# Kernel tuning notes

Hardware: AMD Instinct MI355X
Metric: run time of the kernel (lower is better)

Reference implementation:

```python
import jax, jax.numpy as jnp
import numpy as np

D_MODEL = 512
N_HEADS = 8
D_KV = 64
EPS = 1e-6
ROPE_THETA = 10000.0


def _rms_norm(x, w):
    # T5-style RMSNorm: no mean subtraction, no bias, variance in fp32.
    var = jnp.mean(x.astype(jnp.float32) ** 2, axis=-1, keepdims=True)
    return (x * jax.lax.rsqrt(var + EPS)).astype(x.dtype) * w


def _rope_cos_sin(pos, dk):
    # pos: [B, T] int -> cos/sin: [B, 1, T, dk]
    inv_freq = 1.0 / (ROPE_THETA ** (jnp.arange(0, dk, 2, dtype=jnp.float32) / dk))
    ang = pos.astype(jnp.float32)[:, :, None] * inv_freq[None, None, :]  # [B,T,dk/2]
    ang = jnp.concatenate([ang, ang], axis=-1)                            # [B,T,dk]
    return jnp.cos(ang)[:, None], jnp.sin(ang)[:, None]


def _rotate_half(x):
    h = x.shape[-1] // 2
    return jnp.concatenate([-x[..., h:], x[..., :h]], axis=-1)


def _mha(x, mask, wq, wk, wv, wo, pos=None):
    # x: [B, T, D]; mask: [B, H, T, T] additive
    B, T, _ = x.shape
    def proj(w):
        return (x @ w).reshape(B, T, N_HEADS, D_KV).transpose(0, 2, 1, 3)  # [B,H,T,dk]
    q, k, v = proj(wq), proj(wk), proj(wv)
    if pos is not None:
        cos, sin = _rope_cos_sin(pos, D_KV)
        cos, sin = cos.astype(x.dtype), sin.astype(x.dtype)
        q = q * cos + _rotate_half(q) * sin
        k = k * cos + _rotate_half(k) * sin
    scale = 1.0 / np.sqrt(D_KV)
    scores = jnp.einsum('bhqd,bhkd->bhqk', q, k) * scale + mask
    attn = jax.nn.softmax(scores.astype(jnp.float32), axis=-1).astype(scores.dtype)
    out = jnp.einsum('bhqk,bhkd->bhqd', attn, v)
    out = out.transpose(0, 2, 1, 3).reshape(B, T, N_HEADS * D_KV)
    return out @ wo


def setup_inputs() -> dict:
    key = jax.random.key(0)
    ks = jax.random.split(key, 12)
    B, T = 8, 1024
    s = 1.0 / np.sqrt(D_MODEL)
    inp = {
        'h': jax.random.normal(ks[0], (B, T, D_MODEL), dtype=jnp.float32),
        'pos': jnp.broadcast_to(jnp.arange(T, dtype=jnp.int64 if jax.config.jax_enable_x64 else jnp.int32)[None, :], (B, T)),
        't_mask': jnp.zeros((B, N_HEADS, T, T), dtype=jnp.float32),
        'g_mask': jnp.zeros((T, N_HEADS, B, B), dtype=jnp.float32),
        'ln_t_w': jnp.ones((D_MODEL,), dtype=jnp.float32),
        'ln_g_w': jnp.ones((D_MODEL,), dtype=jnp.float32),
    }
    names = ['wq_t', 'wk_t', 'wv_t', 'wo_t', 'wq_g', 'wk_g', 'wv_g', 'wo_g']
    for i, n in enumerate(names):
        inp[n] = jax.random.normal(ks[i + 1], (D_MODEL, D_MODEL), dtype=jnp.float32) * s
    return inp


def reference(h, pos, t_mask, g_mask, ln_t_w, ln_g_w,
              wq_t, wk_t, wv_t, wo_t, wq_g, wk_g, wv_g, wo_g):
    # --- time attention (over T axis, with RoPE) ---
    normed = _rms_norm(h, ln_t_w)
    attn_t = _mha(normed, t_mask, wq_t, wk_t, wv_t, wo_t, pos=pos)
    h = h + attn_t  # dropout p=0 (eval)
    # --- group attention (over B axis, no RoPE) ---
    h = h.transpose(1, 0, 2)  # [T, B, D]
    normed = _rms_norm(h, ln_g_w)
    attn_g = _mha(normed, g_mask, wq_g, wk_g, wv_g, wo_g, pos=None)
    h = h + attn_g
    return h.transpose(1, 0, 2)  # back to [B, T, D]
```

## Files before the change

kernel.cpp:

```cpp
#include <hip/hip_runtime.h>
#include <hip/hip_bf16.h>
#include <math.h>


typedef __bf16 bf16x8 __attribute__((ext_vector_type(8)));
typedef __bf16 bf16x4 __attribute__((ext_vector_type(4)));
typedef float  f32x4  __attribute__((ext_vector_type(4)));

#define LN1E4_OVER_32 0.2878231366242558f

__device__ __forceinline__ void gld16(const void* g, void* l) {
    __builtin_amdgcn_global_load_lds((const __attribute__((address_space(1))) void*)g,
                                     (__attribute__((address_space(3))) void*)l,
                                     16, 0, 0);
}

__device__ __forceinline__ int swz64(int r, int c) {
    return r * 64 + (((c + r) & 7) << 3);
}

__global__ __launch_bounds__(256) void prep_k(
    const float* __restrict__ x, const float* __restrict__ wln, __bf16* __restrict__ y,
    const float* w0, const float* w1, const float* w2, const float* w3,
    const float* w4, const float* w5, const float* w6, const float* w7,
    const float* __restrict__ gln, float* __restrict__ rmsbuf,
    __bf16* qkvT_t, __bf16* oT_t, __bf16* qkvT_g, __bf16* oT_g,
    const int* __restrict__ pos, float2* __restrict__ rope)
{
    __shared__ float tile[32][33];
    int bid = blockIdx.x;
    if (bid < 2048) {
        if (bid < 32) rmsbuf[bid * 256 + threadIdx.x] = 0.0f;
        int row = bid * 4 + (threadIdx.x >> 6);
        int l = threadIdx.x & 63;
        const float* xr = x + (size_t)row * 512 + l * 8;
        float4 a = *(const float4*)xr;
        float4 b = *(const float4*)(xr + 4);
        float ss = a.x*a.x + a.y*a.y + a.z*a.z + a.w*a.w
                 + b.x*b.x + b.y*b.y + b.z*b.z + b.w*b.w;
        for (int m = 1; m < 64; m <<= 1) ss += __shfl_xor(ss, m);
        float rms = rsqrtf(ss * (1.0f / 512.0f) + 1e-6f);
        float4 wa = *(const float4*)(wln + l * 8);
        float4 wb = *(const float4*)(wln + l * 8 + 4);
        bf16x8 o;
        o[0] = (__bf16)(a.x * rms * wa.x); o[1] = (__bf16)(a.y * rms * wa.y);
        o[2] = (__bf16)(a.z * rms * wa.z); o[3] = (__bf16)(a.w * rms * wa.w);
        o[4] = (__bf16)(b.x * rms * wb.x); o[5] = (__bf16)(b.y * rms * wb.y);
        o[6] = (__bf16)(b.z * rms * wb.z); o[7] = (__bf16)(b.w * rms * wb.w);
        *(bf16x8*)(y + (size_t)row * 512 + l * 8) = o;
        return;
    }
    if (bid >= 4096) {
        int idx = bid - 4096;
        int r = threadIdx.x >> 5, i = threadIdx.x & 31;
        int row = idx * 8 + r;
        float p = (float)pos[row];
        float f = __expf((float)i * -LN1E4_OVER_32);
        float s, c;
        __sincosf(p * f, &s, &c);
        rope[(size_t)row * 32 + i] = make_float2(c, s);
        return;
    }
    int bid2 = bid - 2048;
    int mat = bid2 >> 8, rem = bid2 & 255;
    const float* src; __bf16* dst; int rowOff;
    switch (mat) {
        case 0: src=w0; dst=qkvT_t; rowOff=0;    break;
        case 1: src=w1; dst=qkvT_t; rowOff=512;  break;
        case 2: src=w2; dst=qkvT_t; rowOff=1024; break;
        case 3: src=w3; dst=oT_t;   rowOff=0;    break;
        case 4: src=w4; dst=qkvT_g; rowOff=0;    break;
        case 5: src=w5; dst=qkvT_g; rowOff=512;  break;
        case 6: src=w6; dst=qkvT_g; rowOff=1024; break;
        default: src=w7; dst=oT_g;  rowOff=0;    break;
    }
    bool foldG = (mat >= 4 && mat <= 6);
    int n0 = (rem & 15) * 32, k0 = (rem >> 4) * 32;
    int tt = threadIdx.x;
    int kr = tt >> 3, nc = (tt & 7) * 4;
    float4 v = *(const float4*)(src + (size_t)(k0 + kr) * 512 + n0 + nc);
    tile[kr][nc+0] = v.x; tile[kr][nc+1] = v.y; tile[kr][nc+2] = v.z; tile[kr][nc+3] = v.w;
    __syncthreads();
    int nr = tt >> 3, kc = (tt & 7) * 4;
    float g0 = 1.f, g1 = 1.f, g2 = 1.f, g3 = 1.f;
    if (foldG) {
        float4 gv = *(const float4*)(gln + k0 + kc);
        g0 = gv.x; g1 = gv.y; g2 = gv.z; g3 = gv.w;
    }
    bf16x4 o;
    o[0] = (__bf16)(tile[kc+0][nr] * g0); o[1] = (__bf16)(tile[kc+1][nr] * g1);
    o[2] = (__bf16)(tile[kc+2][nr] * g2); o[3] = (__bf16)(tile[kc+3][nr] * g3);
    *(bf16x4*)(dst + (size_t)(rowOff + n0 + nr) * 512 + k0 + kc) = o;
}

__global__ __launch_bounds__(256) void gemm_ep(
    const __bf16* __restrict__ A, const __bf16* __restrict__ Bt,
    const float2* __restrict__ rope, const float* __restrict__ rmsv,
    __bf16* __restrict__ o0, __bf16* __restrict__ o1, __bf16* __restrict__ o2,
    int mode)
{
    __shared__ __bf16 smem[16384];
    __bf16* As = smem;
    __bf16* Bs = smem + 8192;
    int tid = threadIdx.x;
    int l = tid & 63, w = tid >> 6;
    int l16 = l & 15, quad = l >> 4;
    int wm = w >> 1, wn = w & 1;
    int mblk = blockIdx.x * 128, nblk = blockIdx.y * 128;
    f32x4 acc[4][4] = {};

    for (int k0 = 0; k0 < 512; k0 += 64) {
        __syncthreads();
        #pragma unroll
        for (int i = 0; i < 4; ++i) {
            int idx = i * 256 + tid;
            int row = idx >> 3, cp = idx & 7;
            int cl = (cp - row) & 7;
            gld16(A  + (size_t)(mblk + row) * 512 + k0 + cl * 8, (char*)As + (size_t)idx * 16);
            gld16(Bt + (size_t)(nblk + row) * 512 + k0 + cl * 8, (char*)Bs + (size_t)idx * 16);
        }
        __syncthreads();
        #pragma unroll
        for (int h = 0; h < 2; h++) {
            bf16x8 aF[4], bF[4];
            #pragma unroll
            for (int mt = 0; mt < 4; mt++) aF[mt] = *(bf16x8*)(As + swz64(wm * 64 + mt * 16 + l16, h * 4 + quad));
            #pragma unroll
            for (int nt = 0; nt < 4; nt++) bF[nt] = *(bf16x8*)(Bs + swz64(wn * 64 + nt * 16 + l16, h * 4 + quad));
            #pragma unroll
            for (int mt = 0; mt < 4; mt++)
                #pragma unroll
                for (int nt = 0; nt < 4; nt++)
                    acc[mt][nt] = __builtin_amdgcn_mfma_f32_16x16x32_bf16(aF[mt], bF[nt], acc[mt][nt], 0, 0, 0);
        }
    }
    __syncthreads();

    int colbase = nblk + wn * 64;
    __bf16* bw = smem + w * 1536;
    int rbrow = l >> 3, rbch = (l & 7) * 8;

    int mat = colbase >> 9;
    int hh  = (colbase & 511) >> 6;
    __bf16* dst = (mat == 0) ? o0 : (mat == 1) ? o1 : o2;
    bool isQ = (mat == 0), isV = (mat == 2);
    if (mode == 0 && !isV) {
        #pragma unroll
        for (int mt = 0; mt < 4; mt++) {
            int grow0 = mblk + wm * 64 + mt * 16;
            int b = grow0 >> 10, t0 = grow0 & 1023;
            #pragma unroll
            for (int r = 0; r < 4; r++) {
                const float2* tp = rope + (size_t)(grow0 + quad * 4 + r) * 32;
                #pragma unroll
                for (int nt = 0; nt < 2; nt++) {
                    int i = nt * 16 + l16;
                    float2 cs = tp[i];
                    float x1 = acc[mt][nt][r], x2 = acc[mt][nt + 2][r];
                    float y1 = x1 * cs.x - x2 * cs.y;
                    float y2 = x2 * cs.x + x1 * cs.y;
                    if (isQ) { y1 *= 0.125f; y2 *= 0.125f; }
                    bw[(quad * 4 + r) * 72 + i]      = (__bf16)y1;
                    bw[(quad * 4 + r) * 72 + i + 32] = (__bf16)y2;
                }
            }
            #pragma unroll
            for (int i = 0; i < 2; ++i) {
                int rr = rbrow + i * 8;
                bf16x8 vv = *(bf16x8*)&bw[rr * 72 + rbch];
                *(bf16x8*)&dst[((size_t)(b * 8 + hh) * 1024 + t0 + rr) * 64 + rbch] = vv;
            }
        }
    } else if (mode == 0) {
        #pragma unroll
        for (int mt = 0; mt < 4; mt++) {
            #pragma unroll
            for (int nt = 0; nt < 4; nt++) {
                bf16x4 o4;
                #pragma unroll
                for (int r = 0; r < 4; r++) o4[r] = (__bf16)acc[mt][nt][r];
                *(bf16x4*)&bw[(nt * 16 + l16) * 24 + quad * 4] = o4;
            }
            int grow0 = mblk + wm * 64 + mt * 16;
            int b = grow0 >> 10, t0 = grow0 & 1023;
            #pragma unroll
            for (int i = 0; i < 2; ++i) {
                int li = i * 64 + l;
                int d = li >> 1, t8 = (li & 1) * 8;
                bf16x8 vv = *(bf16x8*)&bw[d * 24 + t8];
                *(bf16x8*)&dst[((size_t)(b * 8 + hh) * 64 + d) * 1024 + t0 + t8] = vv;
            }
        }
    } else {
        #pragma unroll
        for (int mt = 0; mt < 4; mt++) {
            int grow0 = mblk + wm * 64 + mt * 16;
            f32x4 ss4 = *(const f32x4*)&rmsv[grow0 + quad * 4];
            float rsq[4];
            #pragma unroll
            for (int r = 0; r < 4; r++)
                rsq[r] = rsqrtf(ss4[r] * (1.0f / 512.0f) + 1e-6f) * (isQ ? 0.125f : 1.0f);
            #pragma unroll
            for (int nt = 0; nt < 4; nt++)
                #pragma unroll
                for (int r = 0; r < 4; r++)
                    bw[(quad * 4 + r) * 72 + nt * 16 + l16] = (__bf16)(acc[mt][nt][r] * rsq[r]);
            #pragma unroll
            for (int i = 0; i < 2; ++i) {
                int rr = rbrow + i * 8;
                int grow = grow0 + rr;
                int t = grow >> 3, bq = grow & 7;
                bf16x8 vv = *(bf16x8*)&bw[rr * 72 + rbch];
                *(bf16x8*)&dst[(((size_t)t * 8 + hh) * 8 + bq) * 64 + rbch] = vv;
            }
        }
    }
}

__global__ __launch_bounds__(256) void gemm_o(
    const __bf16* __restrict__ A, const __bf16* __restrict__ Bt,
    const float* __restrict__ resid, float* __restrict__ outF,
    __bf16* __restrict__ h2b, float* __restrict__ rmsbuf, int remap)
{
    __shared__ __align__(16) char smemraw[24576];
    __bf16* As = (__bf16*)smemraw;
    __bf16* Bs = (__bf16*)(smemraw + 8192);
    int tid = threadIdx.x;
    int l = tid & 63, w = tid >> 6;
    int l16 = l & 15, quad = l >> 4;
    int mblk = blockIdx.x * 64, nblk = blockIdx.y * 128;
    f32x4 acc[8] = {};

    for (int k0 = 0; k0 < 512; k0 += 64) {
        __syncthreads();
        #pragma unroll
        for (int i = 0; i < 2; ++i) {
            int idx = i * 256 + tid;
            int row = idx >> 3, cp = idx & 7;
            int cl = (cp - row) & 7;
            gld16(A + (size_t)(mblk + row) * 512 + k0 + cl * 8, (char*)As + (size_t)idx * 16);
        }
        #pragma unroll
        for (int i = 0; i < 4; ++i) {
            int idx = i * 256 + tid;
            int row = idx >> 3, cp = idx & 7;
            int cl = (cp - row) & 7;
            gld16(Bt + (size_t)(nblk + row) * 512 + k0 + cl * 8, (char*)Bs + (size_t)idx * 16);
        }
        __syncthreads();
        #pragma unroll
        for (int h = 0; h < 2; h++) {
            bf16x8 aF = *(bf16x8*)(As + swz64(w * 16 + l16, h * 4 + quad));
            #pragma unroll
            for (int nt = 0; nt < 8; nt++) {
                bf16x8 bF = *(bf16x8*)(Bs + swz64(nt * 16 + l16, h * 4 + quad));
                acc[nt] = __builtin_amdgcn_mfma_f32_16x16x32_bf16(aF, bF, acc[nt], 0, 0, 0);
            }
        }
    }
    __syncthreads();

    float* fw = (float*)(smemraw + w * 4352);
    int grow0 = mblk + w * 16;
    float ssq[4] = {0.f, 0.f, 0.f, 0.f};
    #pragma unroll
    for (int nh = 0; nh < 2; nh++) {
        #pragma unroll
        for (int nt = 0; nt < 4; nt++)
            #pragma unroll
            for (int r = 0; r < 4; r++)
                fw[(quad * 4 + r) * 68 + nt * 16 + l16] = acc[nh * 4 + nt][r];
        #pragma unroll
        for (int i = 0; i < 4; ++i) {
            int rr = i * 4 + (l >> 4);
            int c4 = (l & 15) * 4;
            f32x4 a4 = *(f32x4*)&fw[rr * 68 + c4];
            int grow = grow0 + rr;
            int orow = remap ? (((grow & 7) << 10) + (grow >> 3)) : grow;
            size_t oi = (size_t)orow * 512 + nblk + nh * 64 + c4;
            f32x4 r4 = *(const f32x4*)&resid[oi];
            r4 += a4;
            *(f32x4*)&outF[oi] = r4;
            if (!remap) {
                int b = grow >> 10, t = grow & 1023;
                int orow2 = t * 8 + b;
                bf16x4 h4;
                h4[0] = (__bf16)r4[0]; h4[1] = (__bf16)r4[1];
                h4[2] = (__bf16)r4[2]; h4[3] = (__bf16)r4[3];
                *(bf16x4*)&h2b[(size_t)orow2 * 512 + nblk + nh * 64 + c4] = h4;
                ssq[i] += r4[0]*r4[0] + r4[1]*r4[1] + r4[2]*r4[2] + r4[3]*r4[3];
            }
        }
    }
    if (!remap) {
        #pragma unroll
        for (int i = 0; i < 4; ++i) {
            float s = ssq[i];
            s += __shfl_xor(s, 1);
            s += __shfl_xor(s, 2);
            s += __shfl_xor(s, 4);
            s += __shfl_xor(s, 8);
            if ((l & 15) == 0) {
                int grow = grow0 + i * 4 + (l >> 4);
                int orow2 = (grow & 1023) * 8 + (grow >> 10);
                atomicAdd(&rmsbuf[orow2], s);
            }
        }
    }
}

__global__ __launch_bounds__(512) void flash_t(
    const __bf16* __restrict__ q, const __bf16* __restrict__ k,
    const __bf16* __restrict__ vt, const float* __restrict__ tmask,
    __bf16* __restrict__ ctx)
{
    int bh = blockIdx.x;
    int w = threadIdx.x >> 6, l = threadIdx.x & 63;
    int l16 = l & 15, quad = l >> 4;
    int q0 = blockIdx.y * 128 + w * 16;

    __shared__ __bf16 Ks[64 * 72];
    __shared__ __bf16 Vs[64 * 72];
    __shared__ __bf16 Ps[8][16 * 72];

    bf16x8 aQ0, aQ1;
    {
        const __bf16* qp = q + ((size_t)bh * 1024 + q0 + l16) * 64 + quad * 8;
        aQ0 = *(const bf16x8*)qp;
        aQ1 = *(const bf16x8*)(qp + 32);
    }
    f32x4 o[4] = {};
    float l_acc[4] = {0.0f, 0.0f, 0.0f, 0.0f};

    const float* mrow = tmask + (size_t)bh * 1024 * 1024 + (size_t)(q0 + quad * 4) * 1024 + l16;
    float mc[16];
    #pragma unroll
    for (int r = 0; r < 4; r++)
        #pragma unroll
        for (int nt = 0; nt < 4; nt++)
            mc[r * 4 + nt] = __builtin_nontemporal_load(mrow + (size_t)r * 1024 + nt * 16);

    int c = threadIdx.x;
    int srow = c >> 3, scol = (c & 7) << 3;
    const __bf16* kbase = k  + ((size_t)bh * 1024 + srow) * 64 + scol;
    const __bf16* vbase = vt + ((size_t)bh * 64 + srow) * 1024 + scol;
    bf16x8 kreg = *(const bf16x8*)kbase;
    bf16x8 vreg = *(const bf16x8*)vbase;

    for (int jb = 0; jb < 1024; jb += 64) {
        __syncthreads();
        *(bf16x8*)&Ks[srow * 72 + scol] = kreg;
        *(bf16x8*)&Vs[srow * 72 + scol] = vreg;
        __syncthreads();
        if (jb + 64 < 1024) {
            kreg = *(const bf16x8*)(kbase + (size_t)(jb + 64) * 64);
            vreg = *(const bf16x8*)(vbase + (jb + 64));
        }

        float mn_[16];
        {
            int jb2 = (jb + 64) & 1023;
            const float* mr2 = mrow + jb2;
            #pragma unroll
            for (int r = 0; r < 4; r++)
                #pragma unroll
                for (int nt = 0; nt < 4; nt++)
                    mn_[r * 4 + nt] = __builtin_nontemporal_load(mr2 + (size_t)r * 1024 + nt * 16);
        }

        f32x4 s[4] = {};
        #pragma unroll
        for (int nt = 0; nt < 4; nt++) {
            bf16x8 b0 = *(bf16x8*)&Ks[(nt * 16 + l16) * 72 + quad * 8];
            bf16x8 b1 = *(bf16x8*)&Ks[(nt * 16 + l16) * 72 + 32 + quad * 8];
            s[nt] = __builtin_amdgcn_mfma_f32_16x16x32_bf16(aQ0, b0, s[nt], 0, 0, 0);
            s[nt] = __builtin_amdgcn_mfma_f32_16x16x32_bf16(aQ1, b1, s[nt], 0, 0, 0);
        }
        #pragma unroll
        for (int r = 0; r < 4; r++)
            #pragma unroll
            for (int nt = 0; nt < 4; nt++) {
                float p = __expf(s[nt][r] + mc[r * 4 + nt]);
                s[nt][r] = p;
                l_acc[r] += p;
            }

        __bf16* ps = Ps[w];
        #pragma unroll
        for (int nt = 0; nt < 4; nt++)
            #pragma unroll
            for (int r = 0; r < 4; r++)
                ps[(quad * 4 + r) * 72 + nt * 16 + l16] = (__bf16)s[nt][r];
        bf16x8 aP0 = *(bf16x8*)&ps[l16 * 72 + quad * 8];
        bf16x8 aP1 = *(bf16x8*)&ps[l16 * 72 + 32 + quad * 8];
        #pragma unroll
        for (int dt = 0; dt < 4; dt++) {
            bf16x8 bv0 = *(bf16x8*)&Vs[(dt * 16 + l16) * 72 + quad * 8];
            bf16x8 bv1 = *(bf16x8*)&Vs[(dt * 16 + l16) * 72 + 32 + quad * 8];
            o[dt] = __builtin_amdgcn_mfma_f32_16x16x32_bf16(aP0, bv0, o[dt], 0, 0, 0);
            o[dt] = __builtin_amdgcn_mfma_f32_16x16x32_bf16(aP1, bv1, o[dt], 0, 0, 0);
        }

        #pragma unroll
        for (int i = 0; i < 16; i++) mc[i] = mn_[i];
    }

    float inv_l[4];
    #pragma unroll
    for (int r = 0; r < 4; r++) {
        float rs = l_acc[r];
        rs += __shfl_xor(rs, 1);
        rs += __shfl_xor(rs, 2);
        rs += __shfl_xor(rs, 4);
        rs += __shfl_xor(rs, 8);
        inv_l[r] = 1.0f / rs;
    }

    int b = bh >> 3, h = bh & 7;
    __bf16* ps = Ps[w];
    #pragma unroll
    for (int dt = 0; dt < 4; dt++)
        #pragma unroll
        for (int r = 0; r < 4; r++)
            ps[(quad * 4 + r) * 72 + dt * 16 + l16] = (__bf16)(o[dt][r] * inv_l[r]);
    int rbrow = l >> 3, rbch = (l & 7) * 8;
    #pragma unroll
    for (int i = 0; i < 2; ++i) {
        int rr = rbrow + i * 8;
        bf16x8 vv = *(bf16x8*)&ps[rr * 72 + rbch];
        *(bf16x8*)&ctx[((size_t)b * 1024 + q0 + rr) * 512 + h * 64 + rbch] = vv;
    }
}

__global__ __launch_bounds__(256) void group_attn(
    const __bf16* __restrict__ qg, const __bf16* __restrict__ kg,
    const __bf16* __restrict__ vg, const float* __restrict__ gmask,
    __bf16* __restrict__ ctxg)
{
    int tid = blockIdx.x * 256 + threadIdx.x;
    int t = tid >> 6, h = (tid >> 3) & 7, bq = tid & 7;
    size_t base = ((size_t)t * 8 + h) * 512;

    float qv[64];
    #pragma unroll
    for (int d0 = 0; d0 < 64; d0 += 8) {
        bf16x8 qq = *(const bf16x8*)&qg[base + (size_t)bq * 64 + d0];
        #pragma unroll
        for (int u = 0; u < 8; u++) qv[d0 + u] = (float)qq[u];
    }
    float s[8];
    #pragma unroll
    for (int j = 0; j < 8; j++) {
        float acc = 0.0f;
        #pragma unroll
        for (int d0 = 0; d0 < 64; d0 += 8) {
            bf16x8 kk = *(const bf16x8*)&kg[base + (size_t)j * 64 + d0];
            #pragma unroll
            for (int u = 0; u < 8; u++) acc += qv[d0 + u] * (float)kk[u];
        }
        s[j] = acc + gmask[(((size_t)t * 8 + h) * 8 + bq) * 8 + j];
    }
    float mx = s[0];
    #pragma unroll
    for (int j = 1; j < 8; j++) mx = fmaxf(mx, s[j]);
    float sum = 0.0f;
    #pragma unroll
    for (int j = 0; j < 8; j++) { s[j] = __expf(s[j] - mx); sum += s[j]; }
    float inv = 1.0f / sum;

    #pragma unroll
    for (int d0 = 0; d0 < 64; d0 += 8) {
        float o8[8] = {};
        #pragma unroll
        for (int j = 0; j < 8; j++) {
            bf16x8 vv = *(const bf16x8*)&vg[base + (size_t)j * 64 + d0];
            float pj = s[j];
            #pragma unroll
            for (int u = 0; u < 8; u++) o8[u] += pj * (float)vv[u];
        }
        bf16x8 ob;
        #pragma unroll
        for (int u = 0; u < 8; u++) ob[u] = (__bf16)(o8[u] * inv);
        *(bf16x8*)&ctxg[((size_t)t * 8 + bq) * 512 + h * 64 + d0] = ob;
    }
}

extern "C" void kernel_launch(void* const* d_in, const int* in_sizes, int n_in,
                              void* d_out, int out_size, void* d_ws, size_t ws_size,
                              hipStream_t stream)
{
    const float* h      = (const float*)d_in[0];
    const int*   pos    = (const int*)  d_in[1];
    const float* t_mask = (const float*)d_in[2];
    const float* g_mask = (const float*)d_in[3];
    const float* ln_t_w = (const float*)d_in[4];
    const float* ln_g_w = (const float*)d_in[5];
    const float* wq_t = (const float*)d_in[6];
    const float* wk_t = (const float*)d_in[7];
    const float* wv_t = (const float*)d_in[8];
    const float* wo_t = (const float*)d_in[9];
    const float* wq_g = (const float*)d_in[10];
    const float* wk_g = (const float*)d_in[11];
    const float* wv_g = (const float*)d_in[12];
    const float* wo_g = (const float*)d_in[13];
    float* out = (float*)d_out;

    char* ws = (char*)d_ws;
    const size_t MB = 1ull << 20;
    __bf16* qkvT_t = (__bf16*)ws;
    __bf16* oT_t   = qkvT_t + 786432;
    __bf16* qkvT_g = qkvT_t + 1048576;
    __bf16* oT_g   = qkvT_t + 1835008;
    __bf16* normed = (__bf16*)(ws + 4 * MB);
    __bf16* qb     = (__bf16*)(ws + 12 * MB);
    __bf16* kb     = (__bf16*)(ws + 20 * MB);
    __bf16* vb     = (__bf16*)(ws + 28 * MB);
    __bf16* ctx    = (__bf16*)(ws + 36 * MB);
    float*  h2     = (float*) (ws + 44 * MB);
    float*  rmsbuf = (float*) (ws + 60 * MB);
    __bf16* h2b    = (__bf16*)(ws + 61 * MB);
    float2* rope   = (float2*)(ws + 70 * MB);

    prep_k<<<5120, 256, 0, stream>>>(h, ln_t_w, normed,
        wq_t, wk_t, wv_t, wo_t, wq_g, wk_g, wv_g, wo_g,
        ln_g_w, rmsbuf, qkvT_t, oT_t, qkvT_g, oT_g, pos, rope);
    gemm_ep<<<dim3(64, 12), 256, 0, stream>>>(normed, qkvT_t, rope, nullptr, qb, kb, vb, 0);
    flash_t<<<dim3(64, 8), 512, 0, stream>>>(qb, kb, vb, t_mask, ctx);
    gemm_o<<<dim3(128, 4), 256, 0, stream>>>(ctx, oT_t, h, h2, h2b, rmsbuf, 0);

    gemm_ep<<<dim3(64, 12), 256, 0, stream>>>(h2b, qkvT_g, nullptr, rmsbuf, qb, kb, vb, 2);
    group_attn<<<256, 256, 0, stream>>>(qb, kb, vb, g_mask, ctx);
    gemm_o<<<dim3(128, 4), 256, 0, stream>>>(ctx, oT_g, h2, out, nullptr, nullptr, 1);
}
```

Measured before the change: 496.7 us.

## Enlarge QKV GEMM tiles with double-buffered LDS pipeline and retile output GEMM

The QKV projection GEMM moves to 256x256 block tiles with 512 threads. It double-buffers 64-wide K slices in LDS, overlapping global-to-LDS loads with MFMA work using explicit vmcnt waits, barriers and s_setprio around the MFMA bursts. The output-projection GEMM switches from 64x128 tiles with 4 warps sharing the N dimension to 128x128 tiles in a 2x2 warp grid, and does the RMS partial-sum reduction per sub-tile with more atomics. Larger tiles cut redundant operand loads, but they also shrink the grids (192 and 256 blocks), which may leave compute units idle. The 128 KB LDS per block also limits occupancy.

```diff
diff --git a/kernel.cpp b/kernel.cpp
--- a/kernel.cpp
+++ b/kernel.cpp
@@ -93,45 +93,82 @@
     *(bf16x4*)(dst + (size_t)(rowOff + n0 + nr) * 512 + k0 + kc) = o;
 }
 
-__global__ __launch_bounds__(256) void gemm_ep(
+__global__ __launch_bounds__(512) void gemm_ep(
     const __bf16* __restrict__ A, const __bf16* __restrict__ Bt,
     const float2* __restrict__ rope, const float* __restrict__ rmsv,
     __bf16* __restrict__ o0, __bf16* __restrict__ o1, __bf16* __restrict__ o2,
     int mode)
 {
-    __shared__ __bf16 smem[16384];
-    __bf16* As = smem;
-    __bf16* Bs = smem + 8192;
+    __shared__ __bf16 smem[65536];
     int tid = threadIdx.x;
     int l = tid & 63, w = tid >> 6;
     int l16 = l & 15, quad = l >> 4;
-    int wm = w >> 1, wn = w & 1;
-    int mblk = blockIdx.x * 128, nblk = blockIdx.y * 128;
-    f32x4 acc[4][4] = {};
-
-    for (int k0 = 0; k0 < 512; k0 += 64) {
-        __syncthreads();
+    int wm = w >> 2, wn = w & 3;
+    int mblk = blockIdx.x * 256, nblk = blockIdx.y * 256;
+    f32x4 acc[8][4] = {};
+
+    auto stage = [&](int kt, int bb) {
+        int k0 = kt * 64;
+        __bf16* As = smem + bb * 32768;
+        __bf16* Bs = As + 16384;
         #pragma unroll
         for (int i = 0; i < 4; ++i) {
-            int idx = i * 256 + tid;
+            int idx = i * 512 + tid;
             int row = idx >> 3, cp = idx & 7;
             int cl = (cp - row) & 7;
-            gld16(A  + (size_t)(mblk + row) * 512 + k0 + cl * 8, (char*)As + (size_t)idx * 16);
+            gld16(A + (size_t)(mblk + row) * 512 + k0 + cl * 8, (char*)As + (size_t)idx * 16);
+        }
+        #pragma unroll
+        for (int i = 0; i < 4; ++i) {
+            int idx = i * 512 + tid;
+            int row = idx >> 3, cp = idx & 7;
+            int cl = (cp - row) & 7;
             gld16(Bt + (size_t)(nblk + row) * 512 + k0 + cl * 8, (char*)Bs + (size_t)idx * 16);
         }
-        __syncthreads();
-        #pragma unroll
-        for (int h = 0; h < 2; h++) {
-            bf16x8 aF[4], bF[4];
-            #pragma unroll
-            for (int mt = 0; mt < 4; mt++) aF[mt] = *(bf16x8*)(As + swz64(wm * 64 + mt * 16 + l16, h * 4 + quad));
-            #pragma unroll
-            for (int nt = 0; nt < 4; nt++) bF[nt] = *(bf16x8*)(Bs + swz64(wn * 64 + nt * 16 + l16, h * 4 + quad));
-            #pragma unroll
-            for (int mt = 0; mt < 4; mt++)
+    };
+
+    stage(0, 0);
+    stage(1, 1);
+    asm volatile("s_waitcnt vmcnt(8)" ::: "memory");
+    __builtin_amdgcn_s_barrier();
+    __builtin_amdgcn_sched_barrier(0);
+
+    #pragma unroll 1
+    for (int t = 0; t < 8; ++t) {
+        const __bf16* As = smem + (t & 1) * 32768;
+        const __bf16* Bs = As + 16384;
+        bf16x8 bF[4][2];
+        #pragma unroll
+        for (int nt = 0; nt < 4; nt++)
+            #pragma unroll
+            for (int h = 0; h < 2; h++)
+                bF[nt][h] = *(const bf16x8*)(Bs + swz64(wn * 64 + nt * 16 + l16, h * 4 + quad));
+        #pragma unroll
+        for (int p = 0; p < 4; p++) {
+            bf16x8 aF[2][2];
+            #pragma unroll
+            for (int m2 = 0; m2 < 2; m2++)
+                #pragma unroll
+                for (int h = 0; h < 2; h++)
+                    aF[m2][h] = *(const bf16x8*)(As + swz64(wm * 128 + (p * 2 + m2) * 16 + l16, h * 4 + quad));
+            __builtin_amdgcn_s_setprio(1);
+            #pragma unroll
+            for (int m2 = 0; m2 < 2; m2++)
                 #pragma unroll
                 for (int nt = 0; nt < 4; nt++)
-                    acc[mt][nt] = __builtin_amdgcn_mfma_f32_16x16x32_bf16(aF[mt], bF[nt], acc[mt][nt], 0, 0, 0);
+                    #pragma unroll
+                    for (int h = 0; h < 2; h++)
+                        acc[p * 2 + m2][nt] = __builtin_amdgcn_mfma_f32_16x16x32_bf16(
+                            aF[m2][h], bF[nt][h], acc[p * 2 + m2][nt], 0, 0, 0);
+            __builtin_amdgcn_s_setprio(0);
+        }
+        __builtin_amdgcn_s_barrier();
+        if (t < 6) stage(t + 2, t & 1);
+        if (t < 7) {
+            if (t < 6) asm volatile("s_waitcnt vmcnt(8)" ::: "memory");
+            else       asm volatile("s_waitcnt vmcnt(0)" ::: "memory");
+            __builtin_amdgcn_s_barrier();
+            __builtin_amdgcn_sched_barrier(0);
         }
     }
     __syncthreads();
@@ -146,8 +183,8 @@
     bool isQ = (mat == 0), isV = (mat == 2);
     if (mode == 0 && !isV) {
         #pragma unroll
-        for (int mt = 0; mt < 4; mt++) {
-            int grow0 = mblk + wm * 64 + mt * 16;
+        for (int mt = 0; mt < 8; mt++) {
+            int grow0 = mblk + wm * 128 + mt * 16;
             int b = grow0 >> 10, t0 = grow0 & 1023;
             #pragma unroll
             for (int r = 0; r < 4; r++) {
@@ -173,7 +210,7 @@
         }
     } else if (mode == 0) {
         #pragma unroll
-        for (int mt = 0; mt < 4; mt++) {
+        for (int mt = 0; mt < 8; mt++) {
             #pragma unroll
             for (int nt = 0; nt < 4; nt++) {
                 bf16x4 o4;
@@ -181,7 +218,7 @@
                 for (int r = 0; r < 4; r++) o4[r] = (__bf16)acc[mt][nt][r];
                 *(bf16x4*)&bw[(nt * 16 + l16) * 24 + quad * 4] = o4;
             }
-            int grow0 = mblk + wm * 64 + mt * 16;
+            int grow0 = mblk + wm * 128 + mt * 16;
             int b = grow0 >> 10, t0 = grow0 & 1023;
             #pragma unroll
             for (int i = 0; i < 2; ++i) {
@@ -193,8 +230,8 @@
         }
     } else {
         #pragma unroll
-        for (int mt = 0; mt < 4; mt++) {
-            int grow0 = mblk + wm * 64 + mt * 16;
+        for (int mt = 0; mt < 8; mt++) {
+            int grow0 = mblk + wm * 128 + mt * 16;
             f32x4 ss4 = *(const f32x4*)&rmsv[grow0 + quad * 4];
             float rsq[4];
             #pragma unroll
@@ -222,54 +259,52 @@
     const float* __restrict__ resid, float* __restrict__ outF,
     __bf16* __restrict__ h2b, float* __restrict__ rmsbuf, int remap)
 {
-    __shared__ __align__(16) char smemraw[24576];
+    __shared__ __align__(16) char smemraw[32768];
     __bf16* As = (__bf16*)smemraw;
-    __bf16* Bs = (__bf16*)(smemraw + 8192);
+    __bf16* Bs = (__bf16*)(smemraw + 16384);
     int tid = threadIdx.x;
     int l = tid & 63, w = tid >> 6;
     int l16 = l & 15, quad = l >> 4;
-    int mblk = blockIdx.x * 64, nblk = blockIdx.y * 128;
-    f32x4 acc[8] = {};
+    int wm = w >> 1, wn = w & 1;
+    int mblk = blockIdx.x * 128, nblk = blockIdx.y * 128;
+    f32x4 acc[4][4] = {};
 
     for (int k0 = 0; k0 < 512; k0 += 64) {
         __syncthreads();
-        #pragma unroll
-        for (int i = 0; i < 2; ++i) {
-            int idx = i * 256 + tid;
-            int row = idx >> 3, cp = idx & 7;
-            int cl = (cp - row) & 7;
-            gld16(A + (size_t)(mblk + row) * 512 + k0 + cl * 8, (char*)As + (size_t)idx * 16);
-        }
         #pragma unroll
         for (int i = 0; i < 4; ++i) {
             int idx = i * 256 + tid;
             int row = idx >> 3, cp = idx & 7;
             int cl = (cp - row) & 7;
+            gld16(A  + (size_t)(mblk + row) * 512 + k0 + cl * 8, (char*)As + (size_t)idx * 16);
             gld16(Bt + (size_t)(nblk + row) * 512 + k0 + cl * 8, (char*)Bs + (size_t)idx * 16);
         }
         __syncthreads();
         #pragma unroll
         for (int h = 0; h < 2; h++) {
-            bf16x8 aF = *(bf16x8*)(As + swz64(w * 16 + l16, h * 4 + quad));
-            #pragma unroll
-            for (int nt = 0; nt < 8; nt++) {
-                bf16x8 bF = *(bf16x8*)(Bs + swz64(nt * 16 + l16, h * 4 + quad));
-                acc[nt] = __builtin_amdgcn_mfma_f32_16x16x32_bf16(aF, bF, acc[nt], 0, 0, 0);
-            }
+            bf16x8 aF[4], bF[4];
+            #pragma unroll
+            for (int mt = 0; mt < 4; mt++) aF[mt] = *(bf16x8*)(As + swz64(wm * 64 + mt * 16 + l16, h * 4 + quad));
+            #pragma unroll
+            for (int nt = 0; nt < 4; nt++) bF[nt] = *(bf16x8*)(Bs + swz64(wn * 64 + nt * 16 + l16, h * 4 + quad));
+            #pragma unroll
+            for (int mt = 0; mt < 4; mt++)
+                #pragma unroll
+                for (int nt = 0; nt < 4; nt++)
+                    acc[mt][nt] = __builtin_amdgcn_mfma_f32_16x16x32_bf16(aF[mt], bF[nt], acc[mt][nt], 0, 0, 0);
         }
     }
     __syncthreads();
 
     float* fw = (float*)(smemraw + w * 4352);
-    int grow0 = mblk + w * 16;
-    float ssq[4] = {0.f, 0.f, 0.f, 0.f};
-    #pragma unroll
-    for (int nh = 0; nh < 2; nh++) {
+    #pragma unroll
+    for (int mt = 0; mt < 4; mt++) {
+        int grow0 = mblk + wm * 64 + mt * 16;
         #pragma unroll
         for (int nt = 0; nt < 4; nt++)
             #pragma unroll
             for (int r = 0; r < 4; r++)
-                fw[(quad * 4 + r) * 68 + nt * 16 + l16] = acc[nh * 4 + nt][r];
+                fw[(quad * 4 + r) * 68 + nt * 16 + l16] = acc[mt][nt][r];
         #pragma unroll
         for (int i = 0; i < 4; ++i) {
             int rr = i * 4 + (l >> 4);
@@ -277,33 +312,24 @@
             f32x4 a4 = *(f32x4*)&fw[rr * 68 + c4];
             int grow = grow0 + rr;
             int orow = remap ? (((grow & 7) << 10) + (grow >> 3)) : grow;
-            size_t oi = (size_t)orow * 512 + nblk + nh * 64 + c4;
+            size_t oi = (size_t)orow * 512 + nblk + wn * 64 + c4;
             f32x4 r4 = *(const f32x4*)&resid[oi];
             r4 += a4;
             *(f32x4*)&outF[oi] = r4;
             if (!remap) {
-                int b = grow >> 10, t = grow & 1023;
-                int orow2 = t * 8 + b;
+                int b = grow >> 10, tt2 = grow & 1023;
+                int orow2 = tt2 * 8 + b;
                 bf16x4 h4;
                 h4[0] = (__bf16)r4[0]; h4[1] = (__bf16)r4[1];
                 h4[2] = (__bf16)r4[2]; h4[3] = (__bf16)r4[3];
-                *(bf16x4*)&h2b[(size_t)orow2 * 512 + nblk + nh * 64 + c4] = h4;
-                ssq[i] += r4[0]*r4[0] + r4[1]*r4[1] + r4[2]*r4[2] + r4[3]*r4[3];
-            }
-        }
-    }
-    if (!remap) {
-        #pragma unroll
-        for (int i = 0; i < 4; ++i) {
-            float s = ssq[i];
-            s += __shfl_xor(s, 1);
-            s += __shfl_xor(s, 2);
-            s += __shfl_xor(s, 4);
-            s += __shfl_xor(s, 8);
-            if ((l & 15) == 0) {
-                int grow = grow0 + i * 4 + (l >> 4);
-                int orow2 = (grow & 1023) * 8 + (grow >> 10);
-                atomicAdd(&rmsbuf[orow2], s);
+                *(bf16x4*)&h2b[(size_t)orow2 * 512 + nblk + wn * 64 + c4] = h4;
+                float s = r4[0]*r4[0] + r4[1]*r4[1] + r4[2]*r4[2] + r4[3]*r4[3];
+                s += __shfl_xor(s, 1);
+                s += __shfl_xor(s, 2);
+                s += __shfl_xor(s, 4);
+                s += __shfl_xor(s, 8);
+                if ((l & 15) == 0)
+                    atomicAdd(&rmsbuf[(grow & 1023) * 8 + (grow >> 10)], s);
             }
         }
     }
@@ -524,11 +550,11 @@
     prep_k<<<5120, 256, 0, stream>>>(h, ln_t_w, normed,
         wq_t, wk_t, wv_t, wo_t, wq_g, wk_g, wv_g, wo_g,
         ln_g_w, rmsbuf, qkvT_t, oT_t, qkvT_g, oT_g, pos, rope);
-    gemm_ep<<<dim3(64, 12), 256, 0, stream>>>(normed, qkvT_t, rope, nullptr, qb, kb, vb, 0);
+    gemm_ep<<<dim3(32, 6), 512, 0, stream>>>(normed, qkvT_t, rope, nullptr, qb, kb, vb, 0);
     flash_t<<<dim3(64, 8), 512, 0, stream>>>(qb, kb, vb, t_mask, ctx);
-    gemm_o<<<dim3(128, 4), 256, 0, stream>>>(ctx, oT_t, h, h2, h2b, rmsbuf, 0);
-
-    gemm_ep<<<dim3(64, 12), 256, 0, stream>>>(h2b, qkvT_g, nullptr, rmsbuf, qb, kb, vb, 2);
+    gemm_o<<<dim3(64, 4), 256, 0, stream>>>(ctx, oT_t, h, h2, h2b, rmsbuf, 0);
+
+    gemm_ep<<<dim3(32, 6), 512, 0, stream>>>(h2b, qkvT_g, nullptr, rmsbuf, qb, kb, vb, 2);
     group_attn<<<256, 256, 0, stream>>>(qb, kb, vb, g_mask, ctx);
-    gemm_o<<<dim3(128, 4), 256, 0, stream>>>(ctx, oT_g, h2, out, nullptr, nullptr, 1);
-}
+    gemm_o<<<dim3(64, 4), 256, 0, stream>>>(ctx, oT_g, h2, out, nullptr, nullptr, 1);
+}
```

Measured after the change: 503.9 us. No clear change (+1.4%).
